# Kernel optimization log

Hardware: AMD Instinct MI355X
Metric: run time of the kernel (lower is better)

The kernel has to match this reference:

```python
import jax, jax.numpy as jnp
import numpy as np
import math

H = 8
D_MODEL = 4096
D_K = D_MODEL // H  # 512; Sk must equal D_K for the im_attn @ value matmul
B, SQ, SK = 4, 2048, 512


def _linear_params(key, fan_in, fan_out):
    kw, kb = jax.random.split(key)
    bound = 1.0 / math.sqrt(fan_in)
    W = jax.random.uniform(kw, (fan_out, fan_in), jnp.float32, -bound, bound)
    b = jax.random.uniform(kb, (fan_out,), jnp.float32, -bound, bound)
    return W, b


def setup_inputs() -> dict:
    key = jax.random.key(0)
    ks = jax.random.split(key, 8)
    query = jax.random.normal(ks[0], (B, SQ, D_MODEL), jnp.float32)
    k_in = jax.random.normal(ks[1], (B, SK, D_MODEL), jnp.float32)
    v_in = jax.random.normal(ks[2], (B, SK, D_MODEL), jnp.float32)
    image_feat = jax.random.normal(ks[3], (B, SK, D_MODEL), jnp.float32)
    W0, b0 = _linear_params(ks[4], D_MODEL, D_MODEL)
    W1, b1 = _linear_params(ks[5], D_MODEL, D_MODEL)
    W2, b2 = _linear_params(ks[6], D_MODEL, D_MODEL)
    W3, b3 = _linear_params(ks[7], D_MODEL, D_MODEL)  # reused for image_feat AND output proj (as in source)
    return {"query": query, "key": k_in, "value": v_in, "image_feat": image_feat,
            "W0": W0, "b0": b0, "W1": W1, "b1": b1, "W2": W2, "b2": b2, "W3": W3, "b3": b3}


def _split_heads(x):
    # [b, s, d_model] -> [b, h, s, d_k]
    b, s, _ = x.shape
    return x.reshape(b, s, H, D_K).transpose(0, 2, 1, 3)


def reference(query, key, value, image_feat, W0, b0, W1, b1, W2, b2, W3, b3):
    q = _split_heads(query @ W0.T + b0)        # [b,h,Sq,d_k]
    k = _split_heads(key @ W1.T + b1)          # [b,h,Sk,d_k]
    v = _split_heads(value @ W2.T + b2)        # [b,h,Sk,d_k]
    imf = _split_heads(image_feat @ W3.T + b3) # [b,h,Sk,d_k]

    scores = jnp.einsum('bhqd,bhkd->bhqk', q, k) / math.sqrt(D_K)  # [b,h,Sq,Sk]
    p_attn = jax.nn.softmax(scores, axis=-1)
    # second-stage attention over feature axis (Sk == d_k so shapes line up)
    im_attn = jax.nn.softmax(jnp.einsum('bhqk,bhkd->bhqd', p_attn, imf), axis=-1)  # [b,h,Sq,d_k]
    x = jnp.einsum('bhqs,bhsd->bhqd', im_attn, v)  # contracts d_k axis of im_attn with Sk axis of v

    x = x.transpose(0, 2, 1, 3).reshape(query.shape[0], -1, H * D_K)  # [b,Sq,d_model]
    return x @ W3.T + b3  # linears[-1] is the same (shared) 4th linear
```

## Files before the change

### kernel.cpp

```cpp
#include <hip/hip_runtime.h>
#include <hip/hip_bf16.h>
#include <stdint.h>

#define B_   4
#define H_   8
#define SQ_  2048
#define SK_  512
#define DM_  4096
#define DK_  512

typedef __bf16 bf16;
typedef __bf16 bf16x8 __attribute__((ext_vector_type(8)));
typedef float  fx4    __attribute__((ext_vector_type(4)));

typedef __attribute__((address_space(1))) void gv_t;
typedef __attribute__((address_space(3))) void lv_t;

__global__ void sniff_dtype(const uint32_t* __restrict__ q, int* __restrict__ flag)
{
    const int l = threadIdx.x;
    int cnt = 0;
    #pragma unroll
    for (int i = 0; i < 4; ++i) {
        const uint32_t u = q[l * 4 + i];
        const int e = (u >> 7) & 0xFF;
        cnt += (e >= 100 && e <= 135) ? 1 : 0;
    }
    #pragma unroll
    for (int s = 1; s < 64; s <<= 1) cnt += __shfl_xor(cnt, s);
    if (l == 0) *flag = (cnt < 150) ? 1 : 0;
}

__global__ __launch_bounds__(256) void cvt_to_bf16(
    const void* __restrict__ in, bf16* __restrict__ out, const int* __restrict__ flagp)
{
    const size_t i = ((size_t)blockIdx.x * 256 + threadIdx.x) * 8;
    if (*flagp) {
        const float4* p = (const float4*)((const float*)in + i);
        const float4 u0 = p[0], u1 = p[1];
        bf16x8 v;
        v[0] = (bf16)u0.x; v[1] = (bf16)u0.y; v[2] = (bf16)u0.z; v[3] = (bf16)u0.w;
        v[4] = (bf16)u1.x; v[5] = (bf16)u1.y; v[6] = (bf16)u1.z; v[7] = (bf16)u1.w;
        *(bf16x8*)(out + i) = v;
    } else {
        *(bf16x8*)(out + i) = *(const bf16x8*)((const bf16*)in + i);
    }
}

__global__ __launch_bounds__(256, 3) void gemm_bt(
    const bf16* __restrict__ A, const bf16* __restrict__ Bt,
    void* __restrict__ Cv, const void* __restrict__ biasv,
    int K, int lda, int ldb, int ldc, float alpha,
    long long sAb, long long sAh, long long sBb, long long sBh,
    long long sCb, long long sCh,
    const int* __restrict__ flagp, int ebits)
{
    __shared__ bf16 sA[128 * 64];
    __shared__ bf16 sB[128 * 64];

    const int fl = ebits ? *flagp : 0;
    const bool bias32 = fl && (ebits & 1);
    const bool c32    = fl && (ebits & 2);

    const int z = blockIdx.z;
    const int bz = z >> 3, hz = z & 7;
    const bf16* Ab = A  + (size_t)bz * sAb + (size_t)hz * sAh;
    const bf16* Bb = Bt + (size_t)bz * sBb + (size_t)hz * sBh;
    const size_t offC = (size_t)bz * sCb + (size_t)hz * sCh;

    const int n0 = blockIdx.x * 128;
    const int m0 = blockIdx.y * 128;

    const int t = threadIdx.x;
    const int w = t >> 6, l = t & 63;
    const int lrow = l >> 3, lcol = l & 7;
    const int wm = (w >> 1) * 64, wn = (w & 1) * 64;
    const int ml = l & 15, quad = l >> 4;

    const bf16* pa[4];
    const bf16* pb[4];
    #pragma unroll
    for (int i = 0; i < 4; ++i) {
        const int c = w * 4 + i;
        const int r = c * 8 + lrow;
        const int jj = lcol ^ (r & 7);
        pa[i] = Ab + (size_t)(m0 + r) * lda + jj * 8;
        pb[i] = Bb + (size_t)(n0 + r) * ldb + jj * 8;
    }

    fx4 acc[4][4];
    const fx4 zero = {0.f, 0.f, 0.f, 0.f};
    #pragma unroll
    for (int i = 0; i < 4; ++i)
        #pragma unroll
        for (int j = 0; j < 4; ++j) acc[i][j] = zero;

    for (int kt = 0; kt < K; kt += 64) {
        #pragma unroll
        for (int i = 0; i < 4; ++i) {
            const int c = w * 4 + i;
            __builtin_amdgcn_global_load_lds((gv_t*)(pa[i] + kt), (lv_t*)(sA + c * 512), 16, 0, 0);
            __builtin_amdgcn_global_load_lds((gv_t*)(pb[i] + kt), (lv_t*)(sB + c * 512), 16, 0, 0);
        }
        __syncthreads();

        #pragma unroll
        for (int kk = 0; kk < 64; kk += 32) {
            bf16x8 af[4], bfr[4];
            const int jbase = (kk >> 3) + quad;
            #pragma unroll
            for (int mi = 0; mi < 4; ++mi) {
                const int r = wm + mi * 16 + ml;
                af[mi] = *(const bf16x8*)&sA[r * 64 + ((jbase ^ (r & 7)) << 3)];
            }
            #pragma unroll
            for (int ni = 0; ni < 4; ++ni) {
                const int r = wn + ni * 16 + ml;
                bfr[ni] = *(const bf16x8*)&sB[r * 64 + ((jbase ^ (r & 7)) << 3)];
            }
            #pragma unroll
            for (int mi = 0; mi < 4; ++mi)
                #pragma unroll
                for (int ni = 0; ni < 4; ++ni)
                    acc[mi][ni] = __builtin_amdgcn_mfma_f32_16x16x32_bf16(
                        af[mi], bfr[ni], acc[mi][ni], 0, 0, 0);
        }
        __syncthreads();
    }

    #pragma unroll
    for (int ni = 0; ni < 4; ++ni) {
        const int cg = n0 + wn + ni * 16 + ml;
        const float bv = biasv ? (bias32 ? ((const float*)biasv)[cg] : (float)((const bf16*)biasv)[cg]) : 0.f;
        #pragma unroll
        for (int mi = 0; mi < 4; ++mi) {
            const int rg = m0 + wm + mi * 16 + quad * 4;
            #pragma unroll
            for (int r = 0; r < 4; ++r) {
                const float val = acc[mi][ni][r] * alpha + bv;
                const size_t idx = offC + (size_t)(rg + r) * ldc + cg;
                if (c32) ((float*)Cv)[idx] = val;
                else     ((bf16*)Cv)[idx] = (bf16)val;
            }
        }
    }
}

#define ISSUE_TILE(tt, bb)                                                        \
    do {                                                                          \
        _Pragma("unroll")                                                         \
        for (int i_ = 0; i_ < 4; ++i_) {                                          \
            const int c_ = w * 4 + i_;                                            \
            __builtin_amdgcn_global_load_lds((gv_t*)(pa[i_] + (size_t)(tt) * 64), \
                (lv_t*)(&sm[bb][0][c_ * 512]), 16, 0, 0);                         \
            __builtin_amdgcn_global_load_lds((gv_t*)(pb[i_] + (size_t)(tt) * 64), \
                (lv_t*)(&sm[bb][1][c_ * 512]), 16, 0, 0);                         \
        }                                                                         \
    } while (0)

__global__ __launch_bounds__(512, 2) void gemm256(
    const bf16* __restrict__ A, const bf16* __restrict__ Bt,
    void* __restrict__ Cv, const void* __restrict__ biasv,
    int K, int lda, int ldb, int ldc, float alpha,
    long long sAb, long long sAh, long long sBb, long long sBh,
    long long sCb, long long sCh,
    const int* __restrict__ flagp, int ebits)
{
    __shared__ bf16 sm[2][2][256 * 64];

    const int fl = ebits ? *flagp : 0;
    const bool bias32 = fl && (ebits & 1);
    const bool c32    = fl && (ebits & 2);

    const int gX = gridDim.x, gY = gridDim.y;
    int idx = (blockIdx.z * gY + blockIdx.y) * gX + blockIdx.x;
    const int nwg = gX * gY * gridDim.z;
    if ((nwg & 7) == 0) idx = (idx & 7) * (nwg >> 3) + (idx >> 3);
    const int bx = idx % gX;
    const int tmpi = idx / gX;
    const int by = tmpi % gY;
    const int z  = tmpi / gY;

    const int bz = z >> 3, hz = z & 7;
    const bf16* Ab = A  + (size_t)bz * sAb + (size_t)hz * sAh;
    const bf16* Bb = Bt + (size_t)bz * sBb + (size_t)hz * sBh;
    const size_t offC = (size_t)bz * sCb + (size_t)hz * sCh;

    const int n0 = bx * 256;
    const int m0 = by * 256;

    const int t  = threadIdx.x;
    const int w  = t >> 6, l = t & 63;
    const int lrow = l >> 3, lcol = l & 7;
    const int wr = w >> 2, wc = w & 3;
    const int R0 = wr * 128, C0 = wc * 64;
    const int ml = l & 15, quad = l >> 4;

    const bf16* pa[4];
    const bf16* pb[4];
    #pragma unroll
    for (int i = 0; i < 4; ++i) {
        const int c = w * 4 + i;
        const int r = c * 8 + lrow;
        const int jj = lcol ^ (r & 7);
        pa[i] = Ab + (size_t)(m0 + r) * lda + jj * 8;
        pb[i] = Bb + (size_t)(n0 + r) * ldb + jj * 8;
    }

    fx4 acc[8][4];
    const fx4 zero = {0.f, 0.f, 0.f, 0.f};
    #pragma unroll
    for (int i = 0; i < 8; ++i)
        #pragma unroll
        for (int j = 0; j < 4; ++j) acc[i][j] = zero;

    const int nt = K >> 6;

    ISSUE_TILE(0, 0);
    ISSUE_TILE(1, 1);
    asm volatile("s_waitcnt vmcnt(8)" ::: "memory");
    asm volatile("s_barrier" ::: "memory");

    for (int tt = 0; tt < nt; ++tt) {
        const int b = tt & 1;
        const bf16* sA = sm[b][0];
        const bf16* sB = sm[b][1];

        #pragma unroll
        for (int q = 0; q < 4; ++q) {
            const int mh = q >> 1, nh = q & 1;
            bf16x8 af[4][2], bfr[2][2];
            #pragma unroll
            for (int im = 0; im < 4; ++im)
                #pragma unroll
                for (int kI = 0; kI < 2; ++kI) {
                    const int fr = R0 + (mh * 4 + im) * 16 + ml;
                    const int j  = kI * 4 + quad;
                    af[im][kI] = *(const bf16x8*)&sA[fr * 64 + ((j ^ (fr & 7)) << 3)];
                }
            #pragma unroll
            for (int in = 0; in < 2; ++in)
                #pragma unroll
                for (int kI = 0; kI < 2; ++kI) {
                    const int fr = C0 + (nh * 2 + in) * 16 + ml;
                    const int j  = kI * 4 + quad;
                    bfr[in][kI] = *(const bf16x8*)&sB[fr * 64 + ((j ^ (fr & 7)) << 3)];
                }
            asm volatile("s_barrier" ::: "memory");
            __builtin_amdgcn_s_setprio(1);
            #pragma unroll
            for (int kI = 0; kI < 2; ++kI)
                #pragma unroll
                for (int im = 0; im < 4; ++im)
                    #pragma unroll
                    for (int in = 0; in < 2; ++in)
                        acc[mh * 4 + im][nh * 2 + in] =
                            __builtin_amdgcn_mfma_f32_16x16x32_bf16(
                                af[im][kI], bfr[in][kI],
                                acc[mh * 4 + im][nh * 2 + in], 0, 0, 0);
            __builtin_amdgcn_s_setprio(0);
            asm volatile("s_barrier" ::: "memory");
        }

        if (tt + 1 >= nt) break;
        if (tt + 2 < nt) {
            ISSUE_TILE(tt + 2, b);
            asm volatile("s_waitcnt vmcnt(8)" ::: "memory");
        } else {
            asm volatile("s_waitcnt vmcnt(0)" ::: "memory");
        }
        asm volatile("s_barrier" ::: "memory");
    }

    #pragma unroll
    for (int ni = 0; ni < 4; ++ni) {
        const int cg = n0 + C0 + ni * 16 + ml;
        const float bv = biasv ? (bias32 ? ((const float*)biasv)[cg] : (float)((const bf16*)biasv)[cg]) : 0.f;
        #pragma unroll
        for (int mi = 0; mi < 8; ++mi) {
            const int rg = m0 + R0 + mi * 16 + quad * 4;
            #pragma unroll
            for (int r = 0; r < 4; ++r) {
                const float val = acc[mi][ni][r] * alpha + bv;
                const size_t idx = offC + (size_t)(rg + r) * ldc + cg;
                if (c32) ((float*)Cv)[idx] = val;
                else     ((bf16*)Cv)[idx] = (bf16)val;
            }
        }
    }
}

__global__ __launch_bounds__(256) void softmax512(bf16* __restrict__ buf)
{
    const int row = blockIdx.x * 4 + (threadIdx.x >> 6);
    const int l = threadIdx.x & 63;
    bf16* p = buf + (size_t)row * 512 + l * 8;
    bf16x8 v = *(const bf16x8*)p;
    float f[8];
    float mx = -1e30f;
    #pragma unroll
    for (int j = 0; j < 8; ++j) {
        f[j] = (float)v[j];
        if (!(fabsf(f[j]) < 1e30f)) f[j] = -1e9f;
        mx = fmaxf(mx, f[j]);
    }
    #pragma unroll
    for (int s = 1; s < 64; s <<= 1) mx = fmaxf(mx, __shfl_xor(mx, s));
    float sum = 0.f;
    #pragma unroll
    for (int j = 0; j < 8; ++j) { f[j] = __expf(f[j] - mx); sum += f[j]; }
    #pragma unroll
    for (int s = 1; s < 64; s <<= 1) sum += __shfl_xor(sum, s);
    const float inv = 1.f / sum;
    #pragma unroll
    for (int j = 0; j < 8; ++j) v[j] = (bf16)(f[j] * inv);
    *(bf16x8*)p = v;
}

__global__ __launch_bounds__(256) void transpose_heads(
    const bf16* __restrict__ in, bf16* __restrict__ out)
{
    __shared__ bf16 tile[32][33];
    const int z = blockIdx.z, b = z >> 3, h = z & 7;
    const int s0 = blockIdx.x * 32, d0 = blockIdx.y * 32;
    const int tx = threadIdx.x, ty = threadIdx.y;
    #pragma unroll
    for (int j = 0; j < 4; ++j) {
        const int s = s0 + ty + j * 8;
        tile[ty + j * 8][tx] = in[(size_t)b * SK_ * DM_ + (size_t)s * DM_ + h * DK_ + d0 + tx];
    }
    __syncthreads();
    #pragma unroll
    for (int j = 0; j < 4; ++j) {
        const int d = d0 + ty + j * 8;
        out[(size_t)z * DK_ * SK_ + (size_t)d * SK_ + s0 + tx] = tile[tx][ty + j * 8];
    }
}

extern "C" void kernel_launch(void* const* d_in, const int* in_sizes, int n_in,
                              void* d_out, int out_size, void* d_ws, size_t ws_size,
                              hipStream_t stream)
{
    const void* query = d_in[0];
    const void* key   = d_in[1];
    const void* value = d_in[2];
    const void* imf   = d_in[3];
    const void* W0 = d_in[4];  const void* b0 = d_in[5];
    const void* W1 = d_in[6];  const void* b1 = d_in[7];
    const void* W2 = d_in[8];  const void* b2 = d_in[9];
    const void* W3 = d_in[10]; const void* b3 = d_in[11];

    bf16* ws    = (bf16*)d_ws;
    int*  flagp = (int*)d_ws;
    bf16* wslot = ws + 8;
    bf16* R     = ws + 8 + 16777216;
    bf16* inbuf = R;
    bf16* vproj = R + 8388608;
    bf16* imfp  = R + 16777216;
    bf16* s1    = R;
    bf16* xcat  = R;

    bf16* obase = (bf16*)d_out;
    bf16* qproj = obase;
    bf16* qbf   = obase + 33554432;
    bf16* kproj = obase + 33554432;
    bf16* vT    = obase + 41943040;
    bf16* imfT  = obase + 50331648;
    bf16* s2    = obase;

    const float inv_sqrt_dk = 0.04419417382415922f;

    sniff_dtype<<<1, 64, 0, stream>>>((const uint32_t*)query, flagp);

    cvt_to_bf16<<<16384, 256, 0, stream>>>(query, qbf, flagp);
    cvt_to_bf16<<<8192, 256, 0, stream>>>(W0, wslot, flagp);
    gemm256<<<dim3(16, 32, 1), 512, 0, stream>>>(qbf, wslot, qproj, b0,
        4096, 4096, 4096, 4096, 1.f, 0,0,0,0,0,0, flagp, 1);
    cvt_to_bf16<<<4096, 256, 0, stream>>>(key, inbuf, flagp);
    cvt_to_bf16<<<8192, 256, 0, stream>>>(W1, wslot, flagp);
    gemm_bt<<<dim3(32, 16, 1), 256, 0, stream>>>(inbuf, wslot, kproj, b1,
        4096, 4096, 4096, 4096, 1.f, 0,0,0,0,0,0, flagp, 1);
    cvt_to_bf16<<<4096, 256, 0, stream>>>(value, inbuf, flagp);
    cvt_to_bf16<<<8192, 256, 0, stream>>>(W2, wslot, flagp);
    gemm_bt<<<dim3(32, 16, 1), 256, 0, stream>>>(inbuf, wslot, vproj, b2,
        4096, 4096, 4096, 4096, 1.f, 0,0,0,0,0,0, flagp, 1);
    cvt_to_bf16<<<4096, 256, 0, stream>>>(imf, inbuf, flagp);
    cvt_to_bf16<<<8192, 256, 0, stream>>>(W3, wslot, flagp);
    gemm_bt<<<dim3(32, 16, 1), 256, 0, stream>>>(inbuf, wslot, imfp, b3,
        4096, 4096, 4096, 4096, 1.f, 0,0,0,0,0,0, flagp, 1);

    transpose_heads<<<dim3(16, 16, 32), dim3(32, 8), 0, stream>>>(vproj, vT);
    transpose_heads<<<dim3(16, 16, 32), dim3(32, 8), 0, stream>>>(imfp, imfT);

    gemm256<<<dim3(2, 8, 32), 512, 0, stream>>>(qproj, kproj, s1, nullptr,
        512, 4096, 4096, 512, inv_sqrt_dk,
        (long long)SQ_*DM_, (long long)DK_, (long long)SK_*DM_, (long long)DK_,
        (long long)H_*SQ_*SK_, (long long)SQ_*SK_, flagp, 0);
    softmax512<<<dim3(16384), 256, 0, stream>>>(s1);
    gemm256<<<dim3(2, 8, 32), 512, 0, stream>>>(s1, imfT, s2, nullptr,
        512, 512, 512, 512, 1.f,
        (long long)H_*SQ_*SK_, (long long)SQ_*SK_, (long long)H_*DK_*SK_, (long long)DK_*SK_,
        (long long)H_*SQ_*SK_, (long long)SQ_*SK_, flagp, 0);
    softmax512<<<dim3(16384), 256, 0, stream>>>(s2);
    gemm256<<<dim3(2, 8, 32), 512, 0, stream>>>(s2, vT, xcat, nullptr,
        512, 512, 512, 4096, 1.f,
        (long long)H_*SQ_*SK_, (long long)SQ_*SK_, (long long)H_*DK_*SK_, (long long)DK_*SK_,
        (long long)SQ_*DM_, (long long)DK_, flagp, 0);
    cvt_to_bf16<<<8192, 256, 0, stream>>>(W3, wslot, flagp);
    gemm256<<<dim3(16, 32, 1), 512, 0, stream>>>(xcat, wslot, d_out, b3,
        4096, 4096, 4096, 4096, 1.f, 0,0,0,0,0,0, flagp, 3);
}
```

Measured before the change: 1.750 ms.

## Interleave global-to-LDS staging with MFMA quarters and reuse register fragments

Restructures the 256x256 bf16 GEMM main loop into an unrolled pair of half-iterations. Each half-iteration splits the next tile's global-to-LDS loads into three chunks issued between the MFMA quarter blocks. The quarters are ordered so A and B fragments held in registers are reused across quarters, which halves the LDS fragment reads per tile. The trade-offs are a prefetch depth of one tile instead of two, a full vmcnt(0) wait at the end of every tile, and more barriers per tile. The loop also now assumes an even number of K tiles.

```diff
diff --git a/kernel.cpp b/kernel.cpp
--- a/kernel.cpp
+++ b/kernel.cpp
@@ -146,16 +146,91 @@
     }
 }
 
-#define ISSUE_TILE(tt, bb)                                                        \
+#define BARRIER   asm volatile("s_barrier" ::: "memory")
+#define LGKM0     asm volatile("s_waitcnt lgkmcnt(0)" ::: "memory")
+#define VM0       asm volatile("s_waitcnt vmcnt(0)" ::: "memory")
+#define SCHED0    __builtin_amdgcn_sched_barrier(0)
+
+#define LDS_FRAG(dst, base, fr, kI)                                               \
+    dst = *(const bf16x8*)&base[(fr) * 64 + ((((kI) * 4 + quad) ^ ((fr) & 7)) << 3)]
+
+#define READ_A(dst, sX, roff)                                                     \
+    _Pragma("unroll")                                                             \
+    for (int im_ = 0; im_ < 4; ++im_)                                             \
+        _Pragma("unroll")                                                         \
+        for (int kI_ = 0; kI_ < 2; ++kI_)                                         \
+            LDS_FRAG(dst[im_][kI_], sX, R0 + (roff) + im_ * 16 + ml, kI_);
+
+#define READ_B(dst, sX, coff)                                                     \
+    _Pragma("unroll")                                                             \
+    for (int in_ = 0; in_ < 2; ++in_)                                             \
+        _Pragma("unroll")                                                         \
+        for (int kI_ = 0; kI_ < 2; ++kI_)                                         \
+            LDS_FRAG(dst[in_][kI_], sX, C0 + (coff) + in_ * 16 + ml, kI_);
+
+#define MFMA_Q(mo, no, afr_, bfr_)                                                \
+    __builtin_amdgcn_s_setprio(1);                                                \
+    _Pragma("unroll")                                                             \
+    for (int kI_ = 0; kI_ < 2; ++kI_)                                             \
+        _Pragma("unroll")                                                         \
+        for (int im_ = 0; im_ < 4; ++im_)                                         \
+            _Pragma("unroll")                                                     \
+            for (int in_ = 0; in_ < 2; ++in_)                                     \
+                acc[(mo) + im_][(no) + in_] =                                     \
+                    __builtin_amdgcn_mfma_f32_16x16x32_bf16(                      \
+                        afr_[im_][kI_], bfr_[in_][kI_],                           \
+                        acc[(mo) + im_][(no) + in_], 0, 0, 0);                    \
+    __builtin_amdgcn_s_setprio(0);
+
+#define STAGE_A(ts, sb)                                                           \
     do {                                                                          \
         _Pragma("unroll")                                                         \
-        for (int i_ = 0; i_ < 4; ++i_) {                                          \
-            const int c_ = w * 4 + i_;                                            \
-            __builtin_amdgcn_global_load_lds((gv_t*)(pa[i_] + (size_t)(tt) * 64), \
-                (lv_t*)(&sm[bb][0][c_ * 512]), 16, 0, 0);                         \
-            __builtin_amdgcn_global_load_lds((gv_t*)(pb[i_] + (size_t)(tt) * 64), \
-                (lv_t*)(&sm[bb][1][c_ * 512]), 16, 0, 0);                         \
-        }                                                                         \
+        for (int h_ = 0; h_ < 2; ++h_)                                            \
+            _Pragma("unroll")                                                     \
+            for (int j_ = 0; j_ < 2; ++j_)                                        \
+                __builtin_amdgcn_global_load_lds(                                 \
+                    (gv_t*)(pA[h_][j_] + (size_t)(ts) * 64),                      \
+                    (lv_t*)(&sm[sb][0][h_ * 8192 + (2 * w + j_) * 512]),          \
+                    16, 0, 0);                                                    \
+    } while (0)
+
+#define STAGE_B(ts, sb, h)                                                        \
+    do {                                                                          \
+        _Pragma("unroll")                                                         \
+        for (int j_ = 0; j_ < 2; ++j_)                                            \
+            __builtin_amdgcn_global_load_lds(                                     \
+                (gv_t*)(pB[h][j_] + (size_t)(ts) * 64),                           \
+                (lv_t*)(&sm[sb][1][(h) * 8192 + (2 * w + j_) * 512]),             \
+                16, 0, 0);                                                        \
+    } while (0)
+
+#define HALF_ITER(cb, ts, sb, dostage)                                            \
+    do {                                                                          \
+        const bf16* sA_ = &sm[cb][0][0];                                          \
+        const bf16* sB_ = &sm[cb][1][0];                                          \
+                                                                          \
+        READ_A(afr, sA_, 0);                                                      \
+        READ_B(b0r, sB_, 0);                                                      \
+        if (dostage) { STAGE_A(ts, sb); }                                         \
+        BARRIER; LGKM0; SCHED0;                                                   \
+        MFMA_Q(0, 0, afr, b0r);                                                   \
+        BARRIER;                                                                  \
+                                                                          \
+        READ_B(b1r, sB_, 32);                                                     \
+        if (dostage) { STAGE_B(ts, sb, 0); }                                      \
+        BARRIER; LGKM0; SCHED0;                                                   \
+        MFMA_Q(0, 2, afr, b1r);                                                   \
+        BARRIER;                                                                  \
+                                                                          \
+        READ_A(afr, sA_, 64);                                                     \
+        if (dostage) { STAGE_B(ts, sb, 1); }                                      \
+        BARRIER; LGKM0; SCHED0;                                                   \
+        MFMA_Q(4, 2, afr, b1r);                                                   \
+        BARRIER;                                                                  \
+                             \
+        MFMA_Q(4, 0, afr, b0r);                                                   \
+        VM0;                                                                      \
+        BARRIER;                                                                  \
     } while (0)
 
 __global__ __launch_bounds__(512, 2) void gemm256(
@@ -196,16 +271,17 @@
     const int R0 = wr * 128, C0 = wc * 64;
     const int ml = l & 15, quad = l >> 4;
 
-    const bf16* pa[4];
-    const bf16* pb[4];
-    #pragma unroll
-    for (int i = 0; i < 4; ++i) {
-        const int c = w * 4 + i;
-        const int r = c * 8 + lrow;
-        const int jj = lcol ^ (r & 7);
-        pa[i] = Ab + (size_t)(m0 + r) * lda + jj * 8;
-        pb[i] = Bb + (size_t)(n0 + r) * ldb + jj * 8;
-    }
+    const bf16* pA[2][2];
+    const bf16* pB[2][2];
+    #pragma unroll
+    for (int h = 0; h < 2; ++h)
+        #pragma unroll
+        for (int j = 0; j < 2; ++j) {
+            const int r = h * 128 + (2 * w + j) * 8 + lrow;
+            const int jj = lcol ^ (r & 7);
+            pA[h][j] = Ab + (size_t)(m0 + r) * lda + jj * 8;
+            pB[h][j] = Bb + (size_t)(n0 + r) * ldb + jj * 8;
+        }
 
     fx4 acc[8][4];
     const fx4 zero = {0.f, 0.f, 0.f, 0.f};
@@ -214,62 +290,20 @@
         #pragma unroll
         for (int j = 0; j < 4; ++j) acc[i][j] = zero;
 
-    const int nt = K >> 6;
-
-    ISSUE_TILE(0, 0);
-    ISSUE_TILE(1, 1);
-    asm volatile("s_waitcnt vmcnt(8)" ::: "memory");
-    asm volatile("s_barrier" ::: "memory");
-
-    for (int tt = 0; tt < nt; ++tt) {
-        const int b = tt & 1;
-        const bf16* sA = sm[b][0];
-        const bf16* sB = sm[b][1];
-
-        #pragma unroll
-        for (int q = 0; q < 4; ++q) {
-            const int mh = q >> 1, nh = q & 1;
-            bf16x8 af[4][2], bfr[2][2];
-            #pragma unroll
-            for (int im = 0; im < 4; ++im)
-                #pragma unroll
-                for (int kI = 0; kI < 2; ++kI) {
-                    const int fr = R0 + (mh * 4 + im) * 16 + ml;
-                    const int j  = kI * 4 + quad;
-                    af[im][kI] = *(const bf16x8*)&sA[fr * 64 + ((j ^ (fr & 7)) << 3)];
-                }
-            #pragma unroll
-            for (int in = 0; in < 2; ++in)
-                #pragma unroll
-                for (int kI = 0; kI < 2; ++kI) {
-                    const int fr = C0 + (nh * 2 + in) * 16 + ml;
-                    const int j  = kI * 4 + quad;
-                    bfr[in][kI] = *(const bf16x8*)&sB[fr * 64 + ((j ^ (fr & 7)) << 3)];
-                }
-            asm volatile("s_barrier" ::: "memory");
-            __builtin_amdgcn_s_setprio(1);
-            #pragma unroll
-            for (int kI = 0; kI < 2; ++kI)
-                #pragma unroll
-                for (int im = 0; im < 4; ++im)
-                    #pragma unroll
-                    for (int in = 0; in < 2; ++in)
-                        acc[mh * 4 + im][nh * 2 + in] =
-                            __builtin_amdgcn_mfma_f32_16x16x32_bf16(
-                                af[im][kI], bfr[in][kI],
-                                acc[mh * 4 + im][nh * 2 + in], 0, 0, 0);
-            __builtin_amdgcn_s_setprio(0);
-            asm volatile("s_barrier" ::: "memory");
-        }
-
-        if (tt + 1 >= nt) break;
-        if (tt + 2 < nt) {
-            ISSUE_TILE(tt + 2, b);
-            asm volatile("s_waitcnt vmcnt(8)" ::: "memory");
-        } else {
-            asm volatile("s_waitcnt vmcnt(0)" ::: "memory");
-        }
-        asm volatile("s_barrier" ::: "memory");
+    bf16x8 afr[4][2], b0r[2][2], b1r[2][2];
+
+    const int nt  = K >> 6;
+    const int nit = nt >> 1;
+
+    STAGE_A(0, 0);
+    STAGE_B(0, 0, 0);
+    STAGE_B(0, 0, 1);
+    VM0;
+    BARRIER;
+
+    for (int it = 0; it < nit; ++it) {
+        HALF_ITER(0, 2 * it + 1, 1, true);
+        HALF_ITER(1, 2 * it + 2, 0, (it + 1 < nit));
     }
 
     #pragma unroll
```

Measured after the change: 1.503 ms. 14.1% less time.
